# Optimization experiments

Hardware: AMD Instinct MI355X
Metric: run time of the kernel (lower is better)

The kernel has to match this reference:

```python
import jax, jax.numpy as jnp
import numpy as np

B, S, D, H = 2, 2048, 1024, 16
DH = D // H
MASKED_BIAS = -10000.0


def setup_inputs() -> dict:
    key = jax.random.key(0)
    k1, k2, k3 = jax.random.split(key, 3)
    x = jax.random.normal(k1, (B, S, D), dtype=jnp.float32)
    w_attn = jax.random.normal(k2, (D, 3 * D), dtype=jnp.float32) * 0.02
    b_attn = jnp.zeros((3 * D,), dtype=jnp.float32)
    w_proj = jax.random.normal(k3, (D, D), dtype=jnp.float32) * 0.02
    b_proj = jnp.zeros((D,), dtype=jnp.float32)
    return {"x": x, "w_attn": w_attn, "b_attn": b_attn, "w_proj": w_proj, "b_proj": b_proj}


def reference(x, w_attn, b_attn, w_proj, b_proj):
    # c_attn (Conv1D): [B,S,D] @ [D,3D] + b -> [B,S,3D]
    qkv = x @ w_attn + b_attn
    q, k, v = jnp.split(qkv, 3, axis=-1)

    def split_heads(t):  # [B,S,D] -> [B,H,S,DH]
        return t.reshape(B, S, H, DH).transpose(0, 2, 1, 3)

    q, k, v = split_heads(q), split_heads(k), split_heads(v)

    # scores: [B,H,S,S], scaled by sqrt(head_dim) (value.size(-1))
    scores = jnp.einsum('bhqd,bhkd->bhqk', q, k) / jnp.float32(np.sqrt(DH))

    # causal mask via torch.where against masked_bias (-10000.0), not -inf
    causal = jnp.tril(jnp.ones((S, S), dtype=bool))
    scores = jnp.where(causal, scores, jnp.float32(MASKED_BIAS))

    attn = jax.nn.softmax(scores, axis=-1)  # attn_pdrop = 0 -> dropout is identity
    ctx = jnp.einsum('bhqk,bhkd->bhqd', attn, v)  # [B,H,S,DH]

    # merge heads -> [B,S,D], then c_proj (resid_pdrop = 0)
    ctx = ctx.transpose(0, 2, 1, 3).reshape(B, S, D)
    out = ctx @ w_proj + b_proj
    return out
```

## Files before the change

### kernel.cpp

```cpp
#include <hip/hip_runtime.h>
#include <hip/hip_bf16.h>


#define BB 2
#define SS 2048
#define DD 1024
#define HH 16
#define DHH 64
#define MTOK (BB * SS)
#define N3D (3 * DD)
#define QSCALE 0.18033688f

typedef __attribute__((ext_vector_type(8))) short bf16x8;
typedef __attribute__((ext_vector_type(4))) float f32x4;
typedef __attribute__((ext_vector_type(4))) short short4v;

__device__ __forceinline__ short f2bf(float f) {
  unsigned int x = __float_as_uint(f);
  unsigned int r = (x + 0x7fffu + ((x >> 16) & 1u)) >> 16;
  return (short)r;
}

__device__ __forceinline__ unsigned int cvtpk_bf16(float lo, float hi) {
  unsigned int r;
  asm("v_cvt_pk_bf16_f32 %0, %1, %2" : "=v"(r) : "v"(lo), "v"(hi));
  return r;
}

__device__ __forceinline__ float exp2n(float x) {
  float r;
  asm("v_exp_f32 %0, %1" : "=v"(r) : "v"(x));
  return r;
}

__global__ __launch_bounds__(256) void prep_k(const float* __restrict__ x, short* __restrict__ xb,
                                              const float* __restrict__ wa, short* __restrict__ waT,
                                              const float* __restrict__ wp, short* __restrict__ wpT) {
  __shared__ float t[32][33];
  int bid = blockIdx.x, tid = threadIdx.x;
  if (bid < 1024) {
    int base = bid * 1024 + tid;
#pragma unroll
    for (int j = 0; j < 4; ++j) {
      float4 v = reinterpret_cast<const float4*>(x)[base + 256 * j];
      short4v o;
      o[0] = f2bf(v.x); o[1] = f2bf(v.y); o[2] = f2bf(v.z); o[3] = f2bf(v.w);
      reinterpret_cast<short4v*>(xb)[base + 256 * j] = o;
    }
    return;
  }
  const float* W; short* Wt; int K, N, n0, k0;
  if (bid < 4096) {
    int id = bid - 1024;
    W = wa; Wt = waT; K = 1024; N = 3072;
    n0 = (id % 96) * 32; k0 = (id / 96) * 32;
  } else {
    int id = bid - 4096;
    W = wp; Wt = wpT; K = 1024; N = 1024;
    n0 = (id & 31) * 32; k0 = (id >> 5) * 32;
  }
  int tx = tid & 31, ty = tid >> 5;
#pragma unroll
  for (int i = 0; i < 4; ++i)
    t[ty + 8 * i][tx] = W[(size_t)(k0 + ty + 8 * i) * N + n0 + tx];
  __syncthreads();
#pragma unroll
  for (int i = 0; i < 4; ++i)
    Wt[(size_t)(n0 + ty + 8 * i) * K + k0 + tx] = f2bf(t[tx][ty + 8 * i]);
}

template <int OUTF32, int M, int N, int K>
__global__ __launch_bounds__(256) void gemm128_k(const short* __restrict__ A,
                                                 const short* __restrict__ Bt,
                                                 const float* __restrict__ bias,
                                                 void* __restrict__ Cout,
                                                 short* __restrict__ vtout) {
  __shared__ short As[128 * 64];
  __shared__ short Bs[128 * 64];
  constexpr int NX = N / 128;
  constexpr int NWG = NX * (M / 128);
  constexpr int CHUNK = NWG / 8;
  int tid = threadIdx.x;
  int swz = (blockIdx.x & 7) * CHUNK + (blockIdx.x >> 3);
  int m0 = (swz / NX) * 128, n0 = (swz % NX) * 128;
  int w = tid >> 6, lane = tid & 63;
  int wr = w >> 1, wc = w & 1;
  int ln16 = lane & 15, l16 = lane >> 4;

  f32x4 acc[4][4] = {};

  int lrow0 = w * 32 + (lane >> 3);
  int blk_p = lane & 7;

#pragma unroll 1
  for (int k0 = 0; k0 < K; k0 += 64) {
#pragma unroll
    for (int i = 0; i < 4; ++i) {
      int row_p = lrow0 + i * 8;
      int colE = ((blk_p ^ (row_p & 7)) << 3);
      __builtin_amdgcn_global_load_lds(
          (const __attribute__((address_space(1))) unsigned int*)&A[(size_t)(m0 + row_p) * K + k0 + colE],
          (__attribute__((address_space(3))) unsigned int*)&As[(w * 4 + i) * 512],
          16, 0, 0);
      __builtin_amdgcn_global_load_lds(
          (const __attribute__((address_space(1))) unsigned int*)&Bt[(size_t)(n0 + row_p) * K + k0 + colE],
          (__attribute__((address_space(3))) unsigned int*)&Bs[(w * 4 + i) * 512],
          16, 0, 0);
    }
    __syncthreads();
#pragma unroll
    for (int kk = 0; kk < 2; ++kk) {
      bf16x8 a[4], bfr[4];
#pragma unroll
      for (int mi = 0; mi < 4; ++mi) {
        int row = wr * 64 + mi * 16 + ln16;
        int blk = (kk * 4 + l16) ^ (row & 7);
        a[mi] = *reinterpret_cast<const bf16x8*>(&As[row * 64 + blk * 8]);
      }
#pragma unroll
      for (int ni = 0; ni < 4; ++ni) {
        int row = wc * 64 + ni * 16 + ln16;
        int blk = (kk * 4 + l16) ^ (row & 7);
        bfr[ni] = *reinterpret_cast<const bf16x8*>(&Bs[row * 64 + blk * 8]);
      }
#pragma unroll
      for (int mi = 0; mi < 4; ++mi)
#pragma unroll
        for (int ni = 0; ni < 4; ++ni)
          acc[mi][ni] = __builtin_amdgcn_mfma_f32_16x16x32_bf16(a[mi], bfr[ni], acc[mi][ni], 0, 0, 0);
    }
    __syncthreads();
  }

#pragma unroll
  for (int mi = 0; mi < 4; ++mi)
#pragma unroll
    for (int ni = 0; ni < 4; ++ni)
#pragma unroll
      for (int ri = 0; ri < 4; ++ri) {
        int row = m0 + wr * 64 + mi * 16 + l16 * 4 + ri;
        int col = n0 + wc * 64 + ni * 16 + ln16;
        float v = acc[mi][ni][ri] + bias[col];
        if (OUTF32) {
          reinterpret_cast<float*>(Cout)[(size_t)row * N + col] = v;
        } else {
          if (n0 < DD) v *= QSCALE;
          short bv = f2bf(v);
          if (n0 >= 2 * DD) {
            int bb = row >> 11, s = row & 2047;
            vtout[(size_t)(bb * 1024 + col - 2 * DD) * SS + s] = bv;
          } else {
            reinterpret_cast<short*>(Cout)[(size_t)row * N + col] = bv;
          }
        }
      }
}

#define MASKV -3.0e38f
__global__ __launch_bounds__(512) void flash_attn_k(const short* __restrict__ qkv,
                                                    const short* __restrict__ vt,
                                                    short* __restrict__ ctx) {
  __shared__ __align__(16) char smem[53248];
  short (*Ks)[64][72] = reinterpret_cast<short(*)[64][72]>(smem);
  short (*Vs)[64][72] = reinterpret_cast<short(*)[64][72]>(smem + 18432);
  short* Psr = reinterpret_cast<short*>(smem + 36864);
  float* Od = reinterpret_cast<float*>(smem);
  float* mls = reinterpret_cast<float*>(smem + 17408);
  float* lls = reinterpret_cast<float*>(smem + 17920);

  int tid = threadIdx.x;
  int orig = blockIdx.x;
  int wg = (orig & 7) * 64 + (orig >> 3);
  int bh = wg >> 4;
  int pj = wg & 15;
  int b = bh >> 4, h = bh & 15;
  int wgv = tid >> 6, lane = tid & 63;
  int g = wgv >> 2, wq = wgv & 3;
  int ln16 = lane & 15, l16 = lane >> 4;
  int t8 = tid & 255;
  int tb = tid >> 8;
  int r0 = t8 >> 3, cc0 = (t8 & 7) << 3;
  int psq = (wgv << 10) + (ln16 << 6);

  bf16x8 vone;
#pragma unroll
  for (int j = 0; j < 8; ++j) vone[j] = (short)0x3F80;

  const short* kbase = qkv + (size_t)(b * SS) * N3D + DD + h * DHH;
  const short* vbase = vt + (size_t)(bh * DHH) * SS;

#pragma unroll 1
  for (int ti = 0; ti < 2; ++ti) {
    int qt = ti ? pj : 31 - pj;
    int q0 = qt * 64;

    bf16x8 qf[2];
    {
      const short* qrow = qkv + (size_t)(b * SS + q0 + wq * 16 + ln16) * N3D + h * DHH;
      qf[0] = *reinterpret_cast<const bf16x8*>(qrow + l16 * 8);
      qf[1] = *reinterpret_cast<const bf16x8*>(qrow + 32 + l16 * 8);
    }
    float m_ = -1e30f;
    f32x4 cacc[4] = {};
    f32x4 lacc = {};

    int ns = (qt + 2) >> 1;
    uint4 kr0, kr1, vr0, vr1;
    {
      int kt_s = tb <= qt ? tb : qt;
      kr0 = *reinterpret_cast<const uint4*>(kbase + (size_t)(kt_s * 64 + r0) * N3D + cc0);
      kr1 = *reinterpret_cast<const uint4*>(kbase + (size_t)(kt_s * 64 + r0 + 32) * N3D + cc0);
      vr0 = *reinterpret_cast<const uint4*>(vbase + (size_t)r0 * SS + kt_s * 64 + cc0);
      vr1 = *reinterpret_cast<const uint4*>(vbase + (size_t)(r0 + 32) * SS + kt_s * 64 + cc0);
    }

#pragma unroll 1
    for (int s = 0; s < ns; ++s) {
      *reinterpret_cast<uint4*>(&Ks[tb][r0][cc0]) = kr0;
      *reinterpret_cast<uint4*>(&Ks[tb][r0 + 32][cc0]) = kr1;
      *reinterpret_cast<uint4*>(&Vs[tb][r0][cc0]) = vr0;
      *reinterpret_cast<uint4*>(&Vs[tb][r0 + 32][cc0]) = vr1;
      __syncthreads();

      {
        int kt_n = 2 * (s + 1) + tb;
        if (kt_n > qt) kt_n = qt;
        kr0 = *reinterpret_cast<const uint4*>(kbase + (size_t)(kt_n * 64 + r0) * N3D + cc0);
        kr1 = *reinterpret_cast<const uint4*>(kbase + (size_t)(kt_n * 64 + r0 + 32) * N3D + cc0);
        vr0 = *reinterpret_cast<const uint4*>(vbase + (size_t)r0 * SS + kt_n * 64 + cc0);
        vr1 = *reinterpret_cast<const uint4*>(vbase + (size_t)(r0 + 32) * SS + kt_n * 64 + cc0);
      }

      int kt_c = 2 * s + g;
      if (kt_c <= qt) {
        f32x4 sacc[4] = {};
        __builtin_amdgcn_s_setprio(1);
#pragma unroll
        for (int kk = 0; kk < 2; ++kk)
#pragma unroll
          for (int ni = 0; ni < 4; ++ni) {
            bf16x8 kf = *reinterpret_cast<const bf16x8*>(&Ks[g][ni * 16 + ln16][kk * 32 + l16 * 8]);
            sacc[ni] = __builtin_amdgcn_mfma_f32_16x16x32_bf16(kf, qf[kk], sacc[ni], 0, 0, 0);
          }
        __builtin_amdgcn_s_setprio(0);

        float p[4][4];
        float mx = MASKV;
        if (kt_c == qt) {
          int qg = q0 + wq * 16 + ln16;
#pragma unroll
          for (int ni = 0; ni < 4; ++ni)
#pragma unroll
            for (int ri = 0; ri < 4; ++ri) {
              int kg = kt_c * 64 + ni * 16 + l16 * 4 + ri;
              float v = (kg > qg) ? MASKV : sacc[ni][ri];
              p[ni][ri] = v;
              mx = fmaxf(mx, v);
            }
        } else {
#pragma unroll
          for (int ni = 0; ni < 4; ++ni)
#pragma unroll
            for (int ri = 0; ri < 4; ++ri) {
              p[ni][ri] = sacc[ni][ri];
              mx = fmaxf(mx, sacc[ni][ri]);
            }
        }
        mx = fmaxf(mx, __shfl_xor(mx, 16));
        mx = fmaxf(mx, __shfl_xor(mx, 32));

        int keep = __all(mx <= m_ + 11.5f);
        float mn = m_;
        if (!keep) {
          mn = fmaxf(m_, mx);
          float sc = exp2n(m_ - mn);
          float scr[4];
#pragma unroll
          for (int ri = 0; ri < 4; ++ri) scr[ri] = __shfl(sc, l16 * 4 + ri);
#pragma unroll
          for (int di = 0; di < 4; ++di)
#pragma unroll
            for (int ri = 0; ri < 4; ++ri) cacc[di][ri] *= scr[ri];
#pragma unroll
          for (int ri = 0; ri < 4; ++ri) lacc[ri] *= scr[ri];
          m_ = mn;
        }

#pragma unroll
        for (int ni = 0; ni < 4; ++ni)
#pragma unroll
          for (int ri = 0; ri < 4; ++ri)
            p[ni][ri] = exp2n(p[ni][ri] - mn);

#pragma unroll
        for (int ni = 0; ni < 4; ++ni) {
          uint2 u;
          u.x = cvtpk_bf16(p[ni][0], p[ni][1]);
          u.y = cvtpk_bf16(p[ni][2], p[ni][3]);
          int idx = psq + ((((ni << 1) + (l16 >> 1)) ^ (ln16 & 7)) << 3) + ((l16 & 1) << 2);
          *reinterpret_cast<uint2*>(&Psr[idx]) = u;
        }
        asm volatile("s_waitcnt lgkmcnt(0)" ::: "memory");

        __builtin_amdgcn_s_setprio(1);
#pragma unroll
        for (int kk = 0; kk < 2; ++kk) {
          bf16x8 pa = *reinterpret_cast<const bf16x8*>(
              &Psr[psq + ((((kk << 2) + l16) ^ (ln16 & 7)) << 3)]);
          lacc = __builtin_amdgcn_mfma_f32_16x16x32_bf16(pa, vone, lacc, 0, 0, 0);
#pragma unroll
          for (int di = 0; di < 4; ++di) {
            bf16x8 vb = *reinterpret_cast<const bf16x8*>(&Vs[g][di * 16 + ln16][kk * 32 + l16 * 8]);
            cacc[di] = __builtin_amdgcn_mfma_f32_16x16x32_bf16(pa, vb, cacc[di], 0, 0, 0);
          }
        }
        __builtin_amdgcn_s_setprio(0);
      }
      __syncthreads();
    }

    if (g == 1) {
      if (l16 == 0) mls[wq * 16 + ln16] = m_;
      if (ln16 == 0)
#pragma unroll
        for (int ri = 0; ri < 4; ++ri) lls[wq * 16 + l16 * 4 + ri] = lacc[ri];
#pragma unroll
      for (int di = 0; di < 4; ++di)
#pragma unroll
        for (int ri = 0; ri < 4; ++ri)
          Od[wq * 1040 + (l16 * 4 + ri) * 65 + di * 16 + ln16] = cacc[di][ri];
    }
    __syncthreads();
    if (g == 0) {
      float m1 = mls[wq * 16 + ln16];
      float mM = fmaxf(m_, m1);
      float e0 = exp2n(m_ - mM), e1 = exp2n(m1 - mM);
      float e0r[4], e1r[4], ivr[4];
#pragma unroll
      for (int ri = 0; ri < 4; ++ri) {
        int src = l16 * 4 + ri;
        e0r[ri] = __shfl(e0, src);
        e1r[ri] = __shfl(e1, src);
      }
#pragma unroll
      for (int ri = 0; ri < 4; ++ri) {
        float l1 = lls[wq * 16 + l16 * 4 + ri];
        ivr[ri] = 1.f / (lacc[ri] * e0r[ri] + l1 * e1r[ri]);
      }
#pragma unroll
      for (int di = 0; di < 4; ++di)
#pragma unroll
        for (int ri = 0; ri < 4; ++ri) {
          float a1 = Od[wq * 1040 + (l16 * 4 + ri) * 65 + di * 16 + ln16];
          float o = (cacc[di][ri] * e0r[ri] + a1 * e1r[ri]) * ivr[ri];
          int row = q0 + wq * 16 + l16 * 4 + ri;
          int col = h * DHH + di * 16 + ln16;
          ctx[(size_t)(b * SS + row) * DD + col] = f2bf(o);
        }
    }
    __syncthreads();
  }
}

extern "C" void kernel_launch(void* const* d_in, const int* in_sizes, int n_in,
                              void* d_out, int out_size, void* d_ws, size_t ws_size,
                              hipStream_t stream) {
  const float* x      = (const float*)d_in[0];
  const float* w_attn = (const float*)d_in[1];
  const float* b_attn = (const float*)d_in[2];
  const float* w_proj = (const float*)d_in[3];
  const float* b_proj = (const float*)d_in[4];
  float* out = (float*)d_out;

  char* ws = (char*)d_ws;
  short* xb     = (short*)(ws);
  short* wattnT = (short*)(ws + 8388608);
  short* wprojT = (short*)(ws + 14680064);
  short* qkv    = (short*)(ws + 16777216);
  short* vt     = (short*)(ws + 41943040);
  short* ctx    = (short*)(ws + 50331648);

  prep_k<<<5120, 256, 0, stream>>>(x, xb, w_attn, wattnT, w_proj, wprojT);
  gemm128_k<0, MTOK, N3D, DD><<<(N3D / 128) * (MTOK / 128), 256, 0, stream>>>(
      xb, wattnT, b_attn, qkv, vt);
  flash_attn_k<<<dim3(512), 512, 0, stream>>>(qkv, vt, ctx);
  gemm128_k<1, MTOK, DD, DD><<<(DD / 128) * (MTOK / 128), 256, 0, stream>>>(
      ctx, wprojT, b_proj, out, nullptr);
}
```

Measured before the change: 113.9 us.

## Fuse fp32-to-bf16 conversion of x into the QKV GEMM A-tile load

Drops the separate pass that converted x to bf16 in the prep kernel. The QKV GEMM now loads fp32 x tiles straight into LDS with a swizzled layout and converts them to bf16 with v_cvt_pk_bf16_f32 while building MFMA operands. This removes one read and one write of the 16 MB activation. In exchange the A tile in LDS doubles in size, which raises LDS pressure and may lower occupancy, and every workgroup that shares an M row repeats the conversion.

```diff
diff --git a/kernel.cpp b/kernel.cpp
--- a/kernel.cpp
+++ b/kernel.cpp
@@ -33,29 +33,16 @@
   return r;
 }
 
-__global__ __launch_bounds__(256) void prep_k(const float* __restrict__ x, short* __restrict__ xb,
-                                              const float* __restrict__ wa, short* __restrict__ waT,
+__global__ __launch_bounds__(256) void prep_k(const float* __restrict__ wa, short* __restrict__ waT,
                                               const float* __restrict__ wp, short* __restrict__ wpT) {
   __shared__ float t[32][33];
   int bid = blockIdx.x, tid = threadIdx.x;
-  if (bid < 1024) {
-    int base = bid * 1024 + tid;
-#pragma unroll
-    for (int j = 0; j < 4; ++j) {
-      float4 v = reinterpret_cast<const float4*>(x)[base + 256 * j];
-      short4v o;
-      o[0] = f2bf(v.x); o[1] = f2bf(v.y); o[2] = f2bf(v.z); o[3] = f2bf(v.w);
-      reinterpret_cast<short4v*>(xb)[base + 256 * j] = o;
-    }
-    return;
-  }
   const float* W; short* Wt; int K, N, n0, k0;
-  if (bid < 4096) {
-    int id = bid - 1024;
+  if (bid < 3072) {
     W = wa; Wt = waT; K = 1024; N = 3072;
-    n0 = (id % 96) * 32; k0 = (id / 96) * 32;
+    n0 = (bid % 96) * 32; k0 = (bid / 96) * 32;
   } else {
-    int id = bid - 4096;
+    int id = bid - 3072;
     W = wp; Wt = wpT; K = 1024; N = 1024;
     n0 = (id & 31) * 32; k0 = (id >> 5) * 32;
   }
@@ -69,12 +56,107 @@
     Wt[(size_t)(n0 + ty + 8 * i) * K + k0 + tx] = f2bf(t[tx][ty + 8 * i]);
 }
 
-template <int OUTF32, int M, int N, int K>
-__global__ __launch_bounds__(256) void gemm128_k(const short* __restrict__ A,
-                                                 const short* __restrict__ Bt,
-                                                 const float* __restrict__ bias,
-                                                 void* __restrict__ Cout,
-                                                 short* __restrict__ vtout) {
+__global__ __launch_bounds__(256) void gemm128_qkv_k(const float* __restrict__ X,
+                                                     const short* __restrict__ Bt,
+                                                     const float* __restrict__ bias,
+                                                     short* __restrict__ qkv,
+                                                     short* __restrict__ vtout) {
+  __shared__ float Asf[128 * 64];
+  __shared__ short Bs[128 * 64];
+  constexpr int NX = 24, CHUNK = 96;
+  int tid = threadIdx.x;
+  int swz = (blockIdx.x & 7) * CHUNK + (blockIdx.x >> 3);
+  int m0 = (swz / NX) * 128, n0 = (swz % NX) * 128;
+  int w = tid >> 6, lane = tid & 63;
+  int wr = w >> 1, wc = w & 1;
+  int ln16 = lane & 15, l16 = lane >> 4;
+
+  f32x4 acc[4][4] = {};
+
+  int lrow0 = w * 32 + (lane >> 3);
+  int blk_p = lane & 7;
+  int arow_in = lane >> 4;
+  int ablk = lane & 15;
+
+#pragma unroll 1
+  for (int k0 = 0; k0 < 1024; k0 += 64) {
+#pragma unroll
+    for (int i = 0; i < 8; ++i) {
+      int c = w * 8 + i;
+      int row = c * 4 + arow_in;
+      int colE = ((ablk ^ (row & 15)) << 2);
+      __builtin_amdgcn_global_load_lds(
+          (const __attribute__((address_space(1))) unsigned int*)&X[(size_t)(m0 + row) * 1024 + k0 + colE],
+          (__attribute__((address_space(3))) unsigned int*)&Asf[c * 256],
+          16, 0, 0);
+    }
+#pragma unroll
+    for (int i = 0; i < 4; ++i) {
+      int row_p = lrow0 + i * 8;
+      int colE = ((blk_p ^ (row_p & 7)) << 3);
+      __builtin_amdgcn_global_load_lds(
+          (const __attribute__((address_space(1))) unsigned int*)&Bt[(size_t)(n0 + row_p) * 1024 + k0 + colE],
+          (__attribute__((address_space(3))) unsigned int*)&Bs[(w * 4 + i) * 512],
+          16, 0, 0);
+    }
+    __syncthreads();
+#pragma unroll
+    for (int kk = 0; kk < 2; ++kk) {
+      bf16x8 a[4], bfr[4];
+#pragma unroll
+      for (int mi = 0; mi < 4; ++mi) {
+        int row = wr * 64 + mi * 16 + ln16;
+        int b0 = (kk * 8 + l16 * 2) ^ (row & 15);
+        int b1 = (kk * 8 + l16 * 2 + 1) ^ (row & 15);
+        float4 lo = *reinterpret_cast<const float4*>(&Asf[row * 64 + b0 * 4]);
+        float4 hi = *reinterpret_cast<const float4*>(&Asf[row * 64 + b1 * 4]);
+        uint4 uu;
+        uu.x = cvtpk_bf16(lo.x, lo.y);
+        uu.y = cvtpk_bf16(lo.z, lo.w);
+        uu.z = cvtpk_bf16(hi.x, hi.y);
+        uu.w = cvtpk_bf16(hi.z, hi.w);
+        a[mi] = *reinterpret_cast<bf16x8*>(&uu);
+      }
+#pragma unroll
+      for (int ni = 0; ni < 4; ++ni) {
+        int row = wc * 64 + ni * 16 + ln16;
+        int blk = (kk * 4 + l16) ^ (row & 7);
+        bfr[ni] = *reinterpret_cast<const bf16x8*>(&Bs[row * 64 + blk * 8]);
+      }
+#pragma unroll
+      for (int mi = 0; mi < 4; ++mi)
+#pragma unroll
+        for (int ni = 0; ni < 4; ++ni)
+          acc[mi][ni] = __builtin_amdgcn_mfma_f32_16x16x32_bf16(a[mi], bfr[ni], acc[mi][ni], 0, 0, 0);
+    }
+    __syncthreads();
+  }
+
+#pragma unroll
+  for (int mi = 0; mi < 4; ++mi)
+#pragma unroll
+    for (int ni = 0; ni < 4; ++ni)
+#pragma unroll
+      for (int ri = 0; ri < 4; ++ri) {
+        int row = m0 + wr * 64 + mi * 16 + l16 * 4 + ri;
+        int col = n0 + wc * 64 + ni * 16 + ln16;
+        float v = acc[mi][ni][ri] + bias[col];
+        if (n0 < DD) v *= QSCALE;
+        short bv = f2bf(v);
+        if (n0 >= 2 * DD) {
+          int bb = row >> 11, s = row & 2047;
+          vtout[(size_t)(bb * 1024 + col - 2 * DD) * SS + s] = bv;
+        } else {
+          qkv[(size_t)row * N3D + col] = bv;
+        }
+      }
+}
+
+template <int M, int N, int K>
+__global__ __launch_bounds__(256) void gemm128_proj_k(const short* __restrict__ A,
+                                                      const short* __restrict__ Bt,
+                                                      const float* __restrict__ bias,
+                                                      float* __restrict__ Cout) {
   __shared__ short As[128 * 64];
   __shared__ short Bs[128 * 64];
   constexpr int NX = N / 128;
@@ -140,19 +222,7 @@
       for (int ri = 0; ri < 4; ++ri) {
         int row = m0 + wr * 64 + mi * 16 + l16 * 4 + ri;
         int col = n0 + wc * 64 + ni * 16 + ln16;
-        float v = acc[mi][ni][ri] + bias[col];
-        if (OUTF32) {
-          reinterpret_cast<float*>(Cout)[(size_t)row * N + col] = v;
-        } else {
-          if (n0 < DD) v *= QSCALE;
-          short bv = f2bf(v);
-          if (n0 >= 2 * DD) {
-            int bb = row >> 11, s = row & 2047;
-            vtout[(size_t)(bb * 1024 + col - 2 * DD) * SS + s] = bv;
-          } else {
-            reinterpret_cast<short*>(Cout)[(size_t)row * N + col] = bv;
-          }
-        }
+        Cout[(size_t)row * N + col] = acc[mi][ni][ri] + bias[col];
       }
 }
 
@@ -373,17 +443,14 @@
   float* out = (float*)d_out;
 
   char* ws = (char*)d_ws;
-  short* xb     = (short*)(ws);
   short* wattnT = (short*)(ws + 8388608);
   short* wprojT = (short*)(ws + 14680064);
   short* qkv    = (short*)(ws + 16777216);
   short* vt     = (short*)(ws + 41943040);
   short* ctx    = (short*)(ws + 50331648);
 
-  prep_k<<<5120, 256, 0, stream>>>(x, xb, w_attn, wattnT, w_proj, wprojT);
-  gemm128_k<0, MTOK, N3D, DD><<<(N3D / 128) * (MTOK / 128), 256, 0, stream>>>(
-      xb, wattnT, b_attn, qkv, vt);
+  prep_k<<<4096, 256, 0, stream>>>(w_attn, wattnT, w_proj, wprojT);
+  gemm128_qkv_k<<<768, 256, 0, stream>>>(x, wattnT, b_attn, qkv, vt);
   flash_attn_k<<<dim3(512), 512, 0, stream>>>(qkv, vt, ctx);
-  gemm128_k<1, MTOK, DD, DD><<<(DD / 128) * (MTOK / 128), 256, 0, stream>>>(
-      ctx, wprojT, b_proj, out, nullptr);
-}
+  gemm128_proj_k<MTOK, DD, DD><<<256, 256, 0, stream>>>(ctx, wprojT, b_proj, out);
+}
```

After: 131.4 us. 1.15x slower.
